# Kernel optimization log

Hardware: AMD Instinct MI355X
Metric: run time of the kernel (lower is better)

## Reference

```python
import jax, jax.numpy as jnp
import numpy as np

N_ACTIVE = 200000
GRID = 96
C_IN = 128
C_OUT = 128
K = 27  # 3x3x3 kernel offsets
BN_EPS = 1e-4  # scn.BatchNormalization default eps


def _build_rulebook(rng):
    """Sample N_ACTIVE unique voxels in a GRID^3 volume and build the
    submanifold-conv neighbor table: nbr_idx[k, i] = index of the active
    voxel at offset k from voxel i, or -1 if that site is inactive."""
    total = GRID ** 3
    flat = rng.choice(total, size=N_ACTIVE, replace=False).astype(np.int64)
    # flat -> dense lookup of active index
    lut = np.full(total, -1, dtype=np.int32)
    lut[flat] = np.arange(N_ACTIVE, dtype=np.int32)
    z = flat % GRID
    y = (flat // GRID) % GRID
    x = flat // (GRID * GRID)
    offs = np.array([(dx, dy, dz) for dx in (-1, 0, 1)
                     for dy in (-1, 0, 1) for dz in (-1, 0, 1)], dtype=np.int64)
    nbr = np.full((K, N_ACTIVE), -1, dtype=np.int32)
    for k, (dx, dy, dz) in enumerate(offs):
        nx, ny, nz = x + dx, y + dy, z + dz
        ok = ((nx >= 0) & (nx < GRID) & (ny >= 0) & (ny < GRID)
              & (nz >= 0) & (nz < GRID))
        nflat = np.where(ok, nx * GRID * GRID + ny * GRID + nz, 0)
        hit = np.where(ok, lut[nflat], -1)
        nbr[k] = hit
    return nbr


def setup_inputs() -> dict:
    key = jax.random.key(0)
    k1, k2 = jax.random.split(key)
    rng = np.random.default_rng(0)
    nbr_idx = jnp.asarray(_build_rulebook(rng))  # [27, N] int32
    features = jax.random.normal(k1, (N_ACTIVE, C_IN), dtype=jnp.float32)
    # Kaiming-ish scaled conv weights, one [Cin, Cout] matrix per offset
    W = jax.random.normal(k2, (K, C_IN, C_OUT), dtype=jnp.float32) * (
        1.0 / np.sqrt(K * C_IN))
    gamma = jnp.ones((C_OUT,), dtype=jnp.float32)
    beta = jnp.zeros((C_OUT,), dtype=jnp.float32)
    return {"features": features, "nbr_idx": nbr_idx, "W": W,
            "gamma": gamma, "beta": beta}


def reference(features, nbr_idx, W, gamma, beta):
    # --- Submanifold 3x3x3 convolution (gather -> GEMM -> accumulate) ---
    # Output sites == input sites; for each kernel offset k, gather the
    # neighbor's feature row (zero if inactive) and accumulate g @ W[k].
    out = jnp.zeros((features.shape[0], W.shape[-1]), dtype=features.dtype)
    for k in range(K):  # fixed small loop over 27 kernel offsets
        idx = nbr_idx[k]                         # [N]
        valid = (idx >= 0)
        g = features[jnp.maximum(idx, 0)]        # [N, Cin] irregular gather
        g = jnp.where(valid[:, None], g, 0.0)
        out = out + g @ W[k]                     # [N, Cout]
    # --- BatchNormalization over active sites (training batch stats) ---
    mean = jnp.mean(out, axis=0)
    var = jnp.mean(jnp.square(out - mean), axis=0)
    out = (out - mean) * (gamma * jax.lax.rsqrt(var + BN_EPS)) + beta
    # --- ReLU ---
    return jnp.maximum(out, 0.0)
```

## Files before the change

### kernel.cpp

```cpp
#include <hip/hip_runtime.h>
#include <hip/hip_bf16.h>
#include <cstdint>
#include <cstddef>

#define N_ACT 200000
#define CH 128
#define NOFF 27
#define TM 128

typedef __bf16 v8bf __attribute__((ext_vector_type(8)));
typedef float v4f __attribute__((ext_vector_type(4)));

__device__ __forceinline__ unsigned short f2bf(float f) {
    union { float f; unsigned int u; } x; x.f = f;
    unsigned int lsb = (x.u >> 16) & 1u;
    x.u += 0x7fffu + lsb;
    return (unsigned short)(x.u >> 16);
}

__device__ __forceinline__ void gload_lds16(const void* g, void* l) {
    __builtin_amdgcn_global_load_lds(
        (const __attribute__((address_space(1))) unsigned int*)g,
        (__attribute__((address_space(3))) unsigned int*)l,
        16, 0, 0);
}
__device__ __forceinline__ void gload_lds4(const void* g, void* l) {
    __builtin_amdgcn_global_load_lds(
        (const __attribute__((address_space(1))) unsigned int*)g,
        (__attribute__((address_space(3))) unsigned int*)l,
        4, 0, 0);
}

__global__ void prep_and_cast(const float* __restrict__ features,
                              const float* __restrict__ W,
                              unsigned short* __restrict__ feat_bf,
                              unsigned short* __restrict__ Wtp,
                              float* __restrict__ stats,
                              float* __restrict__ zpage) {
    int t = threadIdx.x;
    if (blockIdx.x < NOFF) {
        int k = blockIdx.x;
        if (k == 0 && t < 2 * CH) stats[t] = 0.0f;
        if (k == 0 && t < 64) zpage[t] = 0.0f;
        const float* wk = W + (size_t)k * CH * CH;
        for (int g = t; g < 2048; g += 256) {
            int q = g >> 9, r = g & 511;
            int jkk = r >> 6, lane = r & 63;
            int j = jkk >> 2, kk = jkk & 3;
            int lr = lane & 15, quad = lane >> 4;
            int cout = q * 32 + j * 16 + lr;
            int cin0 = kk * 32 + quad * 8;
            unsigned int wbuf[4];
            #pragma unroll
            for (int h = 0; h < 4; ++h) {
                unsigned short lo = f2bf(wk[(size_t)(cin0 + 2*h)     * CH + cout]);
                unsigned short hi = f2bf(wk[(size_t)(cin0 + 2*h + 1) * CH + cout]);
                wbuf[h] = (unsigned)lo | ((unsigned)hi << 16);
            }
            *(uint4*)(Wtp + ((size_t)(k * 4 + q) << 12)
                          + (size_t)(jkk * 64 + lane) * 8)
                = make_uint4(wbuf[0], wbuf[1], wbuf[2], wbuf[3]);
        }
        return;
    }
    const long long total = (long long)N_ACT * CH / 8;
    long long stride = (long long)(gridDim.x - NOFF) * blockDim.x;
    for (long long i = (long long)(blockIdx.x - NOFF) * blockDim.x + t;
         i < total; i += stride) {
        long long base = i * 8;
        const float4* p = (const float4*)(features + base);
        float4 a = p[0], b = p[1];
        unsigned int w0 = (unsigned)f2bf(a.x) | ((unsigned)f2bf(a.y) << 16);
        unsigned int w1 = (unsigned)f2bf(a.z) | ((unsigned)f2bf(a.w) << 16);
        unsigned int w2 = (unsigned)f2bf(b.x) | ((unsigned)f2bf(b.y) << 16);
        unsigned int w3 = (unsigned)f2bf(b.z) | ((unsigned)f2bf(b.w) << 16);
        *(uint4*)(feat_bf + base) = make_uint4(w0, w1, w2, w3);
    }
}

__global__ __launch_bounds__(256, 4) void conv_mfma(
        const unsigned short* __restrict__ feat,
        const int* __restrict__ nbr,
        const unsigned short* __restrict__ Wtp,
        const unsigned short* __restrict__ zpage,
        float* __restrict__ out,
        float* __restrict__ stats) {
    __shared__ __bf16 As[TM * CH];
    __shared__ int idxS[2][TM];

    const int t    = threadIdx.x;
    const int row0 = blockIdx.x * TM;
    const int wid  = t >> 6;
    const int lane = t & 63;
    const int lr   = lane & 15;
    const int quad = lane >> 4;
    const int sc   = lane & 15;
    const int lhi  = lane >> 4;
    const int wv4  = wid * 4;

    v4f acc[8][2];
    #pragma unroll
    for (int i = 0; i < 8; ++i) {
        acc[i][0] = (v4f){0.f, 0.f, 0.f, 0.f};
        acc[i][1] = (v4f){0.f, 0.f, 0.f, 0.f};
    }

    v8bf B[8];

    auto idxDMA = [&](int k, int slot) {
        const int* src = nbr + (size_t)k * N_ACT;
        int r0 = min(row0 + lane,      N_ACT - 1);
        int r1 = min(row0 + 64 + lane, N_ACT - 1);
        gload_lds4(src + r0, &idxS[slot][0]);
        gload_lds4(src + r1, &idxS[slot][64]);
    };
    auto stageA = [&](int slot) {
        #pragma unroll
        for (int p = 0; p < 8; ++p) {
            int row = p * 16 + wv4 + lhi;
            int idx = idxS[slot][row];
            int gch = (sc - row) & 15;
            const unsigned short* src = (idx >= 0)
                ? feat + ((size_t)idx << 7) + gch * 8
                : zpage + gch * 8;
            gload_lds16(src, As + (size_t)(p * 16 + wv4) * CH);
        }
    };
    auto loadB = [&](int k) {
        const unsigned short* base =
            Wtp + ((size_t)(k * 4 + wid) << 12) + (size_t)lane * 8;
        #pragma unroll
        for (int jkk = 0; jkk < 8; ++jkk)
            B[jkk] = *(const v8bf*)(base + jkk * 512);
    };
    auto mfmaPhase = [&]() {
        #pragma unroll
        for (int i = 0; i < 8; ++i) {
            const __bf16* rowp = As + (i * 16 + lr) * CH;
            v8bf a[4];
            #pragma unroll
            for (int kk = 0; kk < 4; ++kk)
                a[kk] = *(const v8bf*)(rowp + (((kk * 4 + quad + lr) & 15) << 3));
            #pragma unroll
            for (int kk = 0; kk < 4; ++kk) {
                acc[i][0] = __builtin_amdgcn_mfma_f32_16x16x32_bf16(
                    a[kk], B[kk], acc[i][0], 0, 0, 0);
                acc[i][1] = __builtin_amdgcn_mfma_f32_16x16x32_bf16(
                    a[kk], B[4 + kk], acc[i][1], 0, 0, 0);
            }
        }
    };

    if (wid == 0) idxDMA(0, 0);
    __syncthreads();
    stageA(0);
    if (wid == 0) idxDMA(1, 1);
    loadB(0);
    __syncthreads();

    #pragma unroll 1
    for (int k = 0; k < NOFF; ++k) {
        mfmaPhase();
        if (k + 1 < NOFF) {
            __syncthreads();
            stageA((k + 1) & 1);
            if (wid == 0 && k + 2 < NOFF) idxDMA(k + 2, k & 1);
            loadB(k + 1);
            __syncthreads();
        }
    }

    float psum[2] = {0.f, 0.f};
    float psq[2]  = {0.f, 0.f};
    #pragma unroll
    for (int i = 0; i < 8; ++i) {
        #pragma unroll
        for (int r = 0; r < 4; ++r) {
            int grow = row0 + i * 16 + quad * 4 + r;
            if (grow < N_ACT) {
                #pragma unroll
                for (int j = 0; j < 2; ++j) {
                    float v = acc[i][j][r];
                    out[(size_t)grow * CH + wid * 32 + j * 16 + lr] = v;
                    psum[j] += v;
                    psq[j]  += v * v;
                }
            }
        }
    }
    #pragma unroll
    for (int j = 0; j < 2; ++j) {
        psum[j] += __shfl_xor(psum[j], 16, 64);
        psq[j]  += __shfl_xor(psq[j], 16, 64);
        psum[j] += __shfl_xor(psum[j], 32, 64);
        psq[j]  += __shfl_xor(psq[j], 32, 64);
    }
    if (quad == 0) {
        #pragma unroll
        for (int j = 0; j < 2; ++j) {
            int c = wid * 32 + j * 16 + lr;
            atomicAdd(&stats[c],      psum[j]);
            atomicAdd(&stats[CH + c], psq[j]);
        }
    }
}

__global__ void bn_relu(const float* __restrict__ conv,
                        const float* __restrict__ stats,
                        const float* __restrict__ gamma,
                        const float* __restrict__ beta,
                        float* __restrict__ out) {
    const long long total = (long long)N_ACT * CH / 4;
    long long tid = (long long)blockIdx.x * blockDim.x + threadIdx.x;
    int c4 = (int)(tid & 31) * 4;
    float sc[4], sh[4];
    const float inv_n = 1.0f / (float)N_ACT;
    #pragma unroll
    for (int j = 0; j < 4; ++j) {
        int c = c4 + j;
        float mean = stats[c] * inv_n;
        float var  = stats[CH + c] * inv_n - mean * mean;
        float s    = gamma[c] * rsqrtf(var + 1e-4f);
        sc[j] = s;
        sh[j] = beta[c] - mean * s;
    }
    long long stride = (long long)gridDim.x * blockDim.x;
    for (long long i = tid; i < total; i += stride) {
        float4 v = ((const float4*)conv)[i];
        float4 o;
        o.x = fmaxf(v.x * sc[0] + sh[0], 0.f);
        o.y = fmaxf(v.y * sc[1] + sh[1], 0.f);
        o.z = fmaxf(v.z * sc[2] + sh[2], 0.f);
        o.w = fmaxf(v.w * sc[3] + sh[3], 0.f);
        ((float4*)out)[i] = o;
    }
}

extern "C" void kernel_launch(void* const* d_in, const int* in_sizes, int n_in,
                              void* d_out, int out_size, void* d_ws, size_t ws_size,
                              hipStream_t stream) {
    const float* features = (const float*)d_in[0];
    const int*   nbr      = (const int*)d_in[1];
    const float* W        = (const float*)d_in[2];
    const float* gamma    = (const float*)d_in[3];
    const float* beta     = (const float*)d_in[4];
    float* outp = (float*)d_out;

    char* ws = (char*)d_ws;
    unsigned short* feat_bf = (unsigned short*)ws;
    unsigned short* Wtp     = (unsigned short*)(ws + 51200000);
    float* conv             = (float*)(ws + 51200000 + 884736);
    float* stats            = (float*)(ws + 51200000 + 884736 + 102400000);
    float* zpage            = stats + 4 * CH;

    prep_and_cast<<<NOFF + 4096, 256, 0, stream>>>(
        features, W, feat_bf, Wtp, stats, zpage);
    conv_mfma<<<(N_ACT + TM - 1) / TM, 256, 0, stream>>>(
        feat_bf, nbr, Wtp, (const unsigned short*)zpage, conv, stats);
    bn_relu<<<4096, 256, 0, stream>>>(conv, stats, gamma, beta, outp);
}
```

Measured before the change: 385.2 us.

## Halve conv row tile and split waves 2x2 over rows and columns

```diff
diff --git a/kernel.cpp b/kernel.cpp
--- a/kernel.cpp
+++ b/kernel.cpp
@@ -6,7 +6,7 @@
 #define N_ACT 200000
 #define CH 128
 #define NOFF 27
-#define TM 128
+#define TM 64
 
 typedef __bf16 v8bf __attribute__((ext_vector_type(8)));
 typedef float v4f __attribute__((ext_vector_type(4)));
@@ -94,29 +94,27 @@
     const int lane = t & 63;
     const int lr   = lane & 15;
     const int quad = lane >> 4;
+    const int wr   = wid >> 1;
+    const int wc   = wid & 1;
     const int sc   = lane & 15;
     const int lhi  = lane >> 4;
     const int wv4  = wid * 4;
 
-    v4f acc[8][2];
-    #pragma unroll
-    for (int i = 0; i < 8; ++i) {
-        acc[i][0] = (v4f){0.f, 0.f, 0.f, 0.f};
-        acc[i][1] = (v4f){0.f, 0.f, 0.f, 0.f};
-    }
-
-    v8bf B[8];
+    v4f acc[2][4];
+    #pragma unroll
+    for (int i = 0; i < 2; ++i)
+        #pragma unroll
+        for (int j = 0; j < 4; ++j)
+            acc[i][j] = (v4f){0.f, 0.f, 0.f, 0.f};
+
+    v8bf B[16];
 
     auto idxDMA = [&](int k, int slot) {
-        const int* src = nbr + (size_t)k * N_ACT;
-        int r0 = min(row0 + lane,      N_ACT - 1);
-        int r1 = min(row0 + 64 + lane, N_ACT - 1);
-        gload_lds4(src + r0, &idxS[slot][0]);
-        gload_lds4(src + r1, &idxS[slot][64]);
+        gload_lds4(nbr + (size_t)k * N_ACT + row0 + lane, &idxS[slot][0]);
     };
     auto stageA = [&](int slot) {
         #pragma unroll
-        for (int p = 0; p < 8; ++p) {
+        for (int p = 0; p < 4; ++p) {
             int row = p * 16 + wv4 + lhi;
             int idx = idxS[slot][row];
             int gch = (sc - row) & 15;
@@ -127,26 +125,30 @@
         }
     };
     auto loadB = [&](int k) {
-        const unsigned short* base =
-            Wtp + ((size_t)(k * 4 + wid) << 12) + (size_t)lane * 8;
-        #pragma unroll
-        for (int jkk = 0; jkk < 8; ++jkk)
-            B[jkk] = *(const v8bf*)(base + jkk * 512);
+        #pragma unroll
+        for (int j = 0; j < 4; ++j) {
+            const unsigned short* base = Wtp
+                + ((size_t)(k * 4 + 2 * wc + (j >> 1)) << 12)
+                + (size_t)(((j & 1) * 4) * 64 + lane) * 8;
+            #pragma unroll
+            for (int kk = 0; kk < 4; ++kk)
+                B[j * 4 + kk] = *(const v8bf*)(base + kk * 512);
+        }
     };
     auto mfmaPhase = [&]() {
         #pragma unroll
-        for (int i = 0; i < 8; ++i) {
-            const __bf16* rowp = As + (i * 16 + lr) * CH;
+        for (int i = 0; i < 2; ++i) {
+            const __bf16* rowp = As + (wr * 32 + i * 16 + lr) * CH;
             v8bf a[4];
             #pragma unroll
             for (int kk = 0; kk < 4; ++kk)
                 a[kk] = *(const v8bf*)(rowp + (((kk * 4 + quad + lr) & 15) << 3));
             #pragma unroll
             for (int kk = 0; kk < 4; ++kk) {
-                acc[i][0] = __builtin_amdgcn_mfma_f32_16x16x32_bf16(
-                    a[kk], B[kk], acc[i][0], 0, 0, 0);
-                acc[i][1] = __builtin_amdgcn_mfma_f32_16x16x32_bf16(
-                    a[kk], B[4 + kk], acc[i][1], 0, 0, 0);
+                #pragma unroll
+                for (int j = 0; j < 4; ++j)
+                    acc[i][j] = __builtin_amdgcn_mfma_f32_16x16x32_bf16(
+                        a[kk], B[j * 4 + kk], acc[i][j], 0, 0, 0);
             }
         }
     };
@@ -170,26 +172,24 @@
         }
     }
 
-    float psum[2] = {0.f, 0.f};
-    float psq[2]  = {0.f, 0.f};
-    #pragma unroll
-    for (int i = 0; i < 8; ++i) {
+    float psum[4] = {0.f, 0.f, 0.f, 0.f};
+    float psq[4]  = {0.f, 0.f, 0.f, 0.f};
+    #pragma unroll
+    for (int i = 0; i < 2; ++i) {
         #pragma unroll
         for (int r = 0; r < 4; ++r) {
-            int grow = row0 + i * 16 + quad * 4 + r;
-            if (grow < N_ACT) {
-                #pragma unroll
-                for (int j = 0; j < 2; ++j) {
-                    float v = acc[i][j][r];
-                    out[(size_t)grow * CH + wid * 32 + j * 16 + lr] = v;
-                    psum[j] += v;
-                    psq[j]  += v * v;
-                }
+            int grow = row0 + wr * 32 + i * 16 + quad * 4 + r;
+            #pragma unroll
+            for (int j = 0; j < 4; ++j) {
+                float v = acc[i][j][r];
+                out[(size_t)grow * CH + wc * 64 + j * 16 + lr] = v;
+                psum[j] += v;
+                psq[j]  += v * v;
             }
         }
     }
     #pragma unroll
-    for (int j = 0; j < 2; ++j) {
+    for (int j = 0; j < 4; ++j) {
         psum[j] += __shfl_xor(psum[j], 16, 64);
         psq[j]  += __shfl_xor(psq[j], 16, 64);
         psum[j] += __shfl_xor(psum[j], 32, 64);
@@ -197,8 +197,8 @@
     }
     if (quad == 0) {
         #pragma unroll
-        for (int j = 0; j < 2; ++j) {
-            int c = wid * 32 + j * 16 + lr;
+        for (int j = 0; j < 4; ++j) {
+            int c = wc * 64 + j * 16 + lr;
             atomicAdd(&stats[c],      psum[j]);
             atomicAdd(&stats[CH + c], psq[j]);
         }
@@ -255,7 +255,7 @@
 
     prep_and_cast<<<NOFF + 4096, 256, 0, stream>>>(
         features, W, feat_bf, Wtp, stats, zpage);
-    conv_mfma<<<(N_ACT + TM - 1) / TM, 256, 0, stream>>>(
+    conv_mfma<<<N_ACT / TM, 256, 0, stream>>>(
         feat_bf, nbr, Wtp, (const unsigned short*)zpage, conv, stats);
     bn_relu<<<4096, 256, 0, stream>>>(conv, stats, gamma, beta, outp);
 }
```

Result: slower. 486.3 us (+26.2%).
